# Optimization experiments

Hardware: AMD Instinct MI355X
Metric: run time of the kernel (lower is better)

Reference implementation:

```python
import jax, jax.numpy as jnp
import numpy as np


def setup_inputs() -> dict:
    key = jax.random.key(0)
    k1, k2 = jax.random.split(key)
    # [1, D, H, W, C] cubic feature volume
    image_features = jax.random.normal(k1, (1, 64, 64, 64, 64), dtype=jnp.float32)
    # [1, N, 3] vertex coords in the original 128^3 volume, in [0, 128)
    graph_features = jax.random.uniform(k2, (1, 200000, 3), dtype=jnp.float32) * 128.0
    return {"image_features": image_features, "graph_features": graph_features}


def reference(image_features, graph_features):
    img = image_features[0]                      # [D, H, W, C]
    H = img.shape[0]
    factor = jnp.float32(128.0 / H)
    x = graph_features[..., -3] / factor         # [B, N]
    y = graph_features[..., -2] / factor
    z = graph_features[..., -1] / factor
    hm1 = jnp.float32(H - 1)
    x1 = jnp.floor(x); x2 = jnp.minimum(jnp.ceil(x), hm1)
    y1 = jnp.floor(y); y2 = jnp.minimum(jnp.ceil(y), hm1)
    z1 = jnp.floor(z); z2 = jnp.minimum(jnp.ceil(z), hm1)

    def gather(ix, iy, iz):
        # [B, N] index arrays -> [B, N, C] gathered features
        return img[ix.astype(jnp.int32), iy.astype(jnp.int32), iz.astype(jnp.int32)]

    wx = (x - x1)[..., None]; wx2 = (x2 - x)[..., None]
    wy = (y - y1)[..., None]; wy2 = (y2 - y)[..., None]
    wz = (z - z1)[..., None]; wz2 = (z2 - z)[..., None]

    # z = z1 plane
    q11 = gather(x1, y1, z1); q21 = gather(x2, y1, z1)
    q12 = gather(x1, y2, z1); q22 = gather(x2, y2, z1)
    lerp_y1 = (q22 * wx + q12 * wx2) * wy + (q21 * wx + q11 * wx2) * wy2

    # z = z2 plane
    q11 = gather(x1, y1, z2); q21 = gather(x2, y1, z2)
    q12 = gather(x1, y2, z2); q22 = gather(x2, y2, z2)
    lerp_y2 = (q22 * wx + q12 * wx2) * wy + (q21 * wx + q11 * wx2) * wy2

    return lerp_y2 * wz + lerp_y1 * wz2          # [B, N, C]
```

## Files before the change

### kernel.cpp

```cpp
#include <hip/hip_runtime.h>


#define NBUCK   4096
#define CAP     128
#define OVCAP   8192
#define HTILE_F4 1024
#define NGB     8192

typedef float __attribute__((ext_vector_type(4))) fx4;

#define GLOBAL_AS __attribute__((address_space(1)))
#define LDS_AS    __attribute__((address_space(3)))

__device__ __forceinline__ void async_copy16(const float4* g, float4* l) {
    __builtin_amdgcn_global_load_lds(
        (const GLOBAL_AS unsigned int*)(const void*)g,
        (LDS_AS unsigned int*)(void*)l, 16, 0, 0);
}

__device__ __forceinline__ float4 f4mul(float4 a, float s) {
    return make_float4(a.x * s, a.y * s, a.z * s, a.w * s);
}
__device__ __forceinline__ float4 f4fma(float4 a, float s, float4 acc) {
    return make_float4(fmaf(a.x, s, acc.x), fmaf(a.y, s, acc.y),
                       fmaf(a.z, s, acc.z), fmaf(a.w, s, acc.w));
}

__global__ __launch_bounds__(256) void scatter_kernel(
    const float* __restrict__ coords, int* __restrict__ counts,
    float4* __restrict__ buckets, float4* __restrict__ overflow, int n)
{
    int p = blockIdx.x * 256 + threadIdx.x;
    if (p >= n) return;
    float xs = coords[3 * p + 0] * 0.5f;
    float ys = coords[3 * p + 1] * 0.5f;
    float zs = coords[3 * p + 2] * 0.5f;
    int vx = (int)floorf(xs), vy = (int)floorf(ys), vz = (int)floorf(zs);
    int bucket = ((vx >> 2) << 8) | ((vy >> 2) << 4) | (vz >> 2);
    int slot = atomicAdd(&counts[bucket], 1);
    float4 v = make_float4(xs, ys, zs, __int_as_float(p));
    if (slot < CAP) {
        buckets[bucket * CAP + slot] = v;
    } else {
        int o = atomicAdd(&counts[NBUCK], 1);
        if (o < OVCAP) overflow[o] = v;
    }
}

__device__ __forceinline__ void lerp_lds_half(
    const float4* __restrict__ cur, float4 cs,
    int bx0, int by0, int bz0, int cvec, int chbase,
    float* __restrict__ out)
{
    float x = cs.x, y = cs.y, z = cs.z;
    int p = __float_as_int(cs.w);

    float fx1 = floorf(x), fx2 = fminf(ceilf(x), 63.0f);
    float fy1 = floorf(y), fy2 = fminf(ceilf(y), 63.0f);
    float fz1 = floorf(z), fz2 = fminf(ceilf(z), 63.0f);

    int ax1 = ((int)fx1 - bx0) * 25, ax2 = ((int)fx2 - bx0) * 25;
    int ay1 = ((int)fy1 - by0) * 5,  ay2 = ((int)fy2 - by0) * 5;
    int lz1 = (int)fz1 - bz0,        lz2 = (int)fz2 - bz0;

    float wx = x - fx1, wxc = fx2 - x;
    float wy = y - fy1, wyc = fy2 - y;
    float wz = z - fz1, wzc = fz2 - z;

    float4 q11 = cur[((ax1 + ay1 + lz1) << 3) + cvec];
    float4 q21 = cur[((ax2 + ay1 + lz1) << 3) + cvec];
    float4 q12 = cur[((ax1 + ay2 + lz1) << 3) + cvec];
    float4 q22 = cur[((ax2 + ay2 + lz1) << 3) + cvec];
    float4 ly1v = f4fma(f4fma(q22, wx, f4mul(q12, wxc)), wy,
                        f4mul(f4fma(q21, wx, f4mul(q11, wxc)), wyc));
    q11 = cur[((ax1 + ay1 + lz2) << 3) + cvec];
    q21 = cur[((ax2 + ay1 + lz2) << 3) + cvec];
    q12 = cur[((ax1 + ay2 + lz2) << 3) + cvec];
    q22 = cur[((ax2 + ay2 + lz2) << 3) + cvec];
    float4 ly2v = f4fma(f4fma(q22, wx, f4mul(q12, wxc)), wy,
                        f4mul(f4fma(q21, wx, f4mul(q11, wxc)), wyc));

    float4 res = f4fma(ly2v, wz, f4mul(ly1v, wzc));
    fx4 r; r.x = res.x; r.y = res.y; r.z = res.z; r.w = res.w;
    __builtin_nontemporal_store(r, (fx4*)out + (p << 4) + chbase + cvec);
}

__device__ __forceinline__ void lerp_global_store(
    const float4* __restrict__ imgv, float4 cs, int cvec,
    float* __restrict__ out)
{
    float x = cs.x, y = cs.y, z = cs.z;
    int p = __float_as_int(cs.w);

    float fx1 = floorf(x), fx2 = fminf(ceilf(x), 63.0f);
    float fy1 = floorf(y), fy2 = fminf(ceilf(y), 63.0f);
    float fz1 = floorf(z), fz2 = fminf(ceilf(z), 63.0f);

    int bx1 = ((int)fx1) << 12, bx2 = ((int)fx2) << 12;
    int by1 = ((int)fy1) << 6,  by2 = ((int)fy2) << 6;
    int iz1 = (int)fz1, iz2 = (int)fz2;

    float wx = x - fx1, wxc = fx2 - x;
    float wy = y - fy1, wyc = fy2 - y;
    float wz = z - fz1, wzc = fz2 - z;

    float4 q11 = imgv[((bx1 + by1 + iz1) << 4) + cvec];
    float4 q21 = imgv[((bx2 + by1 + iz1) << 4) + cvec];
    float4 q12 = imgv[((bx1 + by2 + iz1) << 4) + cvec];
    float4 q22 = imgv[((bx2 + by2 + iz1) << 4) + cvec];
    float4 ly1v = f4fma(f4fma(q22, wx, f4mul(q12, wxc)), wy,
                        f4mul(f4fma(q21, wx, f4mul(q11, wxc)), wyc));
    q11 = imgv[((bx1 + by1 + iz2) << 4) + cvec];
    q21 = imgv[((bx2 + by1 + iz2) << 4) + cvec];
    q12 = imgv[((bx1 + by2 + iz2) << 4) + cvec];
    q22 = imgv[((bx2 + by2 + iz2) << 4) + cvec];
    float4 ly2v = f4fma(f4fma(q22, wx, f4mul(q12, wxc)), wy,
                        f4mul(f4fma(q21, wx, f4mul(q11, wxc)), wyc));

    float4 res = f4fma(ly2v, wz, f4mul(ly1v, wzc));
    fx4 r; r.x = res.x; r.y = res.y; r.z = res.z; r.w = res.w;
    __builtin_nontemporal_store(r, (fx4*)out + (p << 4) + cvec);
}

__global__ __launch_bounds__(256, 8) void gather_kernel(
    const float* __restrict__ img, const int* __restrict__ counts,
    const float4* __restrict__ buckets, const float4* __restrict__ overflow,
    float* __restrict__ out)
{
    const float4* __restrict__ imgv = (const float4*)img;

    if (blockIdx.x < NGB) {
        __shared__ float4 tile[HTILE_F4];
        int cvec = threadIdx.x & 7;
        int grp  = threadIdx.x >> 3;
        int wv   = threadIdx.x >> 6;
        int lane = threadIdx.x & 63;

        int seq    = (blockIdx.x & 7) * 1024 + (blockIdx.x >> 3);
        int bucket = seq >> 1;
        int half   = seq & 1;
        int chbase = half << 3;
        int base   = bucket * CAP;
        int bx0 = (bucket >> 8) << 2;
        int by0 = ((bucket >> 4) & 15) << 2;
        int bz0 = (bucket & 15) << 2;

        int cnt = counts[bucket];
        float4 cs0 = buckets[base + grp];
        float4 cs1 = buckets[base + grp + 32];

        #pragma unroll
        for (int c = 0; c < 4; c++) {
            int chunk = (wv << 2) + c;
            int f = chunk * 64 + lane;
            int tv = min(f >> 3, 124);
            int ch = f & 7;
            int lx = tv / 25;
            int rem = tv - lx * 25;
            int ly = rem / 5;
            int lz = rem - ly * 5;
            int gx = min(bx0 + lx, 63);
            int gy = min(by0 + ly, 63);
            int gz = min(bz0 + lz, 63);
            const float4* src =
                &imgv[(((((gx << 6) + gy) << 6) + gz) << 4) + chbase + ch];
            async_copy16(src, &tile[chunk * 64]);
        }
        cnt = min(cnt, CAP);

        __syncthreads();

        if (grp < cnt)
            lerp_lds_half(tile, cs0, bx0, by0, bz0, cvec, chbase, out);
        if (grp + 32 < cnt)
            lerp_lds_half(tile, cs1, bx0, by0, bz0, cvec, chbase, out);
        for (int t = grp + 64; t < cnt; t += 32) {
            float4 cs = buckets[base + t];
            lerp_lds_half(tile, cs, bx0, by0, bz0, cvec, chbase, out);
        }
    } else {
        int cvec = threadIdx.x & 15;
        int grp  = threadIdx.x >> 4;
        int ob = blockIdx.x - NGB;
        int cnt = min(counts[NBUCK], OVCAP);
        for (int i = (ob << 4) + grp; i < cnt; i += 32 * 16) {
            float4 cs = overflow[i];
            lerp_global_store(imgv, cs, cvec, out);
        }
    }
}

__global__ __launch_bounds__(256) void trilerp_kernel(
    const float* __restrict__ img, const float* __restrict__ coords,
    float* __restrict__ out, int n_points)
{
    int tid = blockIdx.x * 256 + threadIdx.x;
    int p = tid >> 4;
    if (p >= n_points) return;
    int cvec = tid & 15;

    float x = coords[3 * p + 0] * 0.5f;
    float y = coords[3 * p + 1] * 0.5f;
    float z = coords[3 * p + 2] * 0.5f;

    float4 cs = make_float4(x, y, z, __int_as_float(p));
    lerp_global_store((const float4*)img, cs, cvec, out);
}

extern "C" void kernel_launch(void* const* d_in, const int* in_sizes, int n_in,
                              void* d_out, int out_size, void* d_ws, size_t ws_size,
                              hipStream_t stream) {
    const float* img    = (const float*)d_in[0];
    const float* coords = (const float*)d_in[1];
    float* out = (float*)d_out;
    int n = in_sizes[1] / 3;

    size_t counts_bytes = 32768;
    size_t buckets_off  = counts_bytes;
    size_t buckets_bytes = (size_t)NBUCK * CAP * sizeof(float4);
    size_t overflow_off = buckets_off + buckets_bytes;
    size_t need = overflow_off + (size_t)OVCAP * sizeof(float4);

    if (ws_size >= need) {
        int*    counts   = (int*)d_ws;
        float4* buckets  = (float4*)((char*)d_ws + buckets_off);
        float4* overflow = (float4*)((char*)d_ws + overflow_off);

        hipMemsetAsync(counts, 0, (NBUCK + 1) * sizeof(int), stream);
        int pgrid = (n + 255) / 256;
        scatter_kernel<<<pgrid, 256, 0, stream>>>(coords, counts, buckets, overflow, n);
        gather_kernel<<<NGB + 32, 256, 0, stream>>>(img, counts, buckets, overflow, out);
    } else {
        int threads = n * 16;
        int grid = (threads + 255) / 256;
        trilerp_kernel<<<grid, 256, 0, stream>>>(img, coords, out, n);
    }
}
```

Measured before the change: 140.2 us.

## Enlarge spatial buckets to 8^3 voxels with quarter-channel LDS tiles

Points are now binned into 512 buckets of 8^3 voxels instead of 4096 buckets of 4^3. Each 512-thread block loads a 9^3-voxel halo tile for a quarter of the channels into LDS, about 46 KB. The aim is to cut redundant halo reads of the feature volume: the halo ratio drops from 125/64 to 729/512, which lowers global memory traffic for the tile loads. In exchange, fewer and larger blocks use more LDS each, occupancy drops, and there is less overlap between the tile-load phase and the compute phase.

```diff
diff --git a/kernel.cpp b/kernel.cpp
--- a/kernel.cpp
+++ b/kernel.cpp
@@ -1,11 +1,11 @@
 #include <hip/hip_runtime.h>
 
 
-#define NBUCK   4096
-#define CAP     128
+#define NB8     512
+#define CAP8    640
 #define OVCAP   8192
-#define HTILE_F4 1024
-#define NGB     8192
+#define TILE8_F4 2944
+#define NGB     2048
 
 typedef float __attribute__((ext_vector_type(4))) fx4;
 
@@ -36,18 +36,18 @@
     float ys = coords[3 * p + 1] * 0.5f;
     float zs = coords[3 * p + 2] * 0.5f;
     int vx = (int)floorf(xs), vy = (int)floorf(ys), vz = (int)floorf(zs);
-    int bucket = ((vx >> 2) << 8) | ((vy >> 2) << 4) | (vz >> 2);
+    int bucket = ((vx >> 3) << 6) | ((vy >> 3) << 3) | (vz >> 3);
     int slot = atomicAdd(&counts[bucket], 1);
     float4 v = make_float4(xs, ys, zs, __int_as_float(p));
-    if (slot < CAP) {
-        buckets[bucket * CAP + slot] = v;
+    if (slot < CAP8) {
+        buckets[bucket * CAP8 + slot] = v;
     } else {
-        int o = atomicAdd(&counts[NBUCK], 1);
+        int o = atomicAdd(&counts[NB8], 1);
         if (o < OVCAP) overflow[o] = v;
     }
 }
 
-__device__ __forceinline__ void lerp_lds_half(
+__device__ __forceinline__ void lerp_lds_q(
     const float4* __restrict__ cur, float4 cs,
     int bx0, int by0, int bz0, int cvec, int chbase,
     float* __restrict__ out)
@@ -59,24 +59,24 @@
     float fy1 = floorf(y), fy2 = fminf(ceilf(y), 63.0f);
     float fz1 = floorf(z), fz2 = fminf(ceilf(z), 63.0f);
 
-    int ax1 = ((int)fx1 - bx0) * 25, ax2 = ((int)fx2 - bx0) * 25;
-    int ay1 = ((int)fy1 - by0) * 5,  ay2 = ((int)fy2 - by0) * 5;
+    int ax1 = ((int)fx1 - bx0) * 81, ax2 = ((int)fx2 - bx0) * 81;
+    int ay1 = ((int)fy1 - by0) * 9,  ay2 = ((int)fy2 - by0) * 9;
     int lz1 = (int)fz1 - bz0,        lz2 = (int)fz2 - bz0;
 
     float wx = x - fx1, wxc = fx2 - x;
     float wy = y - fy1, wyc = fy2 - y;
     float wz = z - fz1, wzc = fz2 - z;
 
-    float4 q11 = cur[((ax1 + ay1 + lz1) << 3) + cvec];
-    float4 q21 = cur[((ax2 + ay1 + lz1) << 3) + cvec];
-    float4 q12 = cur[((ax1 + ay2 + lz1) << 3) + cvec];
-    float4 q22 = cur[((ax2 + ay2 + lz1) << 3) + cvec];
+    float4 q11 = cur[((ax1 + ay1 + lz1) << 2) + cvec];
+    float4 q21 = cur[((ax2 + ay1 + lz1) << 2) + cvec];
+    float4 q12 = cur[((ax1 + ay2 + lz1) << 2) + cvec];
+    float4 q22 = cur[((ax2 + ay2 + lz1) << 2) + cvec];
     float4 ly1v = f4fma(f4fma(q22, wx, f4mul(q12, wxc)), wy,
                         f4mul(f4fma(q21, wx, f4mul(q11, wxc)), wyc));
-    q11 = cur[((ax1 + ay1 + lz2) << 3) + cvec];
-    q21 = cur[((ax2 + ay1 + lz2) << 3) + cvec];
-    q12 = cur[((ax1 + ay2 + lz2) << 3) + cvec];
-    q22 = cur[((ax2 + ay2 + lz2) << 3) + cvec];
+    q11 = cur[((ax1 + ay1 + lz2) << 2) + cvec];
+    q21 = cur[((ax2 + ay1 + lz2) << 2) + cvec];
+    q12 = cur[((ax1 + ay2 + lz2) << 2) + cvec];
+    q22 = cur[((ax2 + ay2 + lz2) << 2) + cvec];
     float4 ly2v = f4fma(f4fma(q22, wx, f4mul(q12, wxc)), wy,
                         f4mul(f4fma(q21, wx, f4mul(q11, wxc)), wyc));
 
@@ -122,7 +122,7 @@
     __builtin_nontemporal_store(r, (fx4*)out + (p << 4) + cvec);
 }
 
-__global__ __launch_bounds__(256, 8) void gather_kernel(
+__global__ __launch_bounds__(512, 4) void gather_kernel(
     const float* __restrict__ img, const int* __restrict__ counts,
     const float4* __restrict__ buckets, const float4* __restrict__ overflow,
     float* __restrict__ out)
@@ -130,60 +130,65 @@
     const float4* __restrict__ imgv = (const float4*)img;
 
     if (blockIdx.x < NGB) {
-        __shared__ float4 tile[HTILE_F4];
-        int cvec = threadIdx.x & 7;
-        int grp  = threadIdx.x >> 3;
+        __shared__ float4 tile[TILE8_F4];
+        int cvec = threadIdx.x & 3;
+        int grp  = threadIdx.x >> 2;
         int wv   = threadIdx.x >> 6;
         int lane = threadIdx.x & 63;
 
-        int seq    = (blockIdx.x & 7) * 1024 + (blockIdx.x >> 3);
-        int bucket = seq >> 1;
-        int half   = seq & 1;
-        int chbase = half << 3;
-        int base   = bucket * CAP;
-        int bx0 = (bucket >> 8) << 2;
-        int by0 = ((bucket >> 4) & 15) << 2;
-        int bz0 = (bucket & 15) << 2;
+        int seq    = (blockIdx.x & 7) * 256 + (blockIdx.x >> 3);
+        int bucket = seq >> 2;
+        int split  = seq & 3;
+        int chbase = split << 2;
+        int base   = bucket * CAP8;
+        int bx0 = (bucket >> 6) << 3;
+        int by0 = ((bucket >> 3) & 7) << 3;
+        int bz0 = (bucket & 7) << 3;
 
         int cnt = counts[bucket];
         float4 cs0 = buckets[base + grp];
-        float4 cs1 = buckets[base + grp + 32];
+        float4 cs1 = buckets[base + grp + 128];
+        float4 cs2 = buckets[base + grp + 256];
 
         #pragma unroll
-        for (int c = 0; c < 4; c++) {
-            int chunk = (wv << 2) + c;
-            int f = chunk * 64 + lane;
-            int tv = min(f >> 3, 124);
-            int ch = f & 7;
-            int lx = tv / 25;
-            int rem = tv - lx * 25;
-            int ly = rem / 5;
-            int lz = rem - ly * 5;
-            int gx = min(bx0 + lx, 63);
-            int gy = min(by0 + ly, 63);
-            int gz = min(bz0 + lz, 63);
-            const float4* src =
-                &imgv[(((((gx << 6) + gy) << 6) + gz) << 4) + chbase + ch];
-            async_copy16(src, &tile[chunk * 64]);
+        for (int c = 0; c < 6; c++) {
+            int chunk = wv * 6 + c;
+            if (chunk < 46) {
+                int f = chunk * 64 + lane;
+                int tv = min(f >> 2, 728);
+                int ch = (f & 3) + chbase;
+                int lx = tv / 81;
+                int rem = tv - lx * 81;
+                int ly = rem / 9;
+                int lz = rem - ly * 9;
+                int gx = min(bx0 + lx, 63);
+                int gy = min(by0 + ly, 63);
+                int gz = min(bz0 + lz, 63);
+                const float4* src =
+                    &imgv[(((((gx << 6) + gy) << 6) + gz) << 4) + ch];
+                async_copy16(src, &tile[chunk * 64]);
+            }
         }
-        cnt = min(cnt, CAP);
+        cnt = min(cnt, CAP8);
 
         __syncthreads();
 
         if (grp < cnt)
-            lerp_lds_half(tile, cs0, bx0, by0, bz0, cvec, chbase, out);
-        if (grp + 32 < cnt)
-            lerp_lds_half(tile, cs1, bx0, by0, bz0, cvec, chbase, out);
-        for (int t = grp + 64; t < cnt; t += 32) {
+            lerp_lds_q(tile, cs0, bx0, by0, bz0, cvec, chbase, out);
+        if (grp + 128 < cnt)
+            lerp_lds_q(tile, cs1, bx0, by0, bz0, cvec, chbase, out);
+        if (grp + 256 < cnt)
+            lerp_lds_q(tile, cs2, bx0, by0, bz0, cvec, chbase, out);
+        for (int t = grp + 384; t < cnt; t += 128) {
             float4 cs = buckets[base + t];
-            lerp_lds_half(tile, cs, bx0, by0, bz0, cvec, chbase, out);
+            lerp_lds_q(tile, cs, bx0, by0, bz0, cvec, chbase, out);
         }
     } else {
         int cvec = threadIdx.x & 15;
         int grp  = threadIdx.x >> 4;
         int ob = blockIdx.x - NGB;
-        int cnt = min(counts[NBUCK], OVCAP);
-        for (int i = (ob << 4) + grp; i < cnt; i += 32 * 16) {
+        int cnt = min(counts[NB8], OVCAP);
+        for (int i = (ob << 5) + grp; i < cnt; i += 32 * 32) {
             float4 cs = overflow[i];
             lerp_global_store(imgv, cs, cvec, out);
         }
@@ -215,10 +220,10 @@
     float* out = (float*)d_out;
     int n = in_sizes[1] / 3;
 
-    size_t counts_bytes = 32768;
-    size_t buckets_off  = counts_bytes;
-    size_t buckets_bytes = (size_t)NBUCK * CAP * sizeof(float4);
-    size_t overflow_off = buckets_off + buckets_bytes;
+    size_t counts_bytes  = 32768;
+    size_t buckets_off   = counts_bytes;
+    size_t buckets_bytes = (size_t)NB8 * CAP8 * sizeof(float4);
+    size_t overflow_off  = buckets_off + buckets_bytes;
     size_t need = overflow_off + (size_t)OVCAP * sizeof(float4);
 
     if (ws_size >= need) {
@@ -226,10 +231,10 @@
         float4* buckets  = (float4*)((char*)d_ws + buckets_off);
         float4* overflow = (float4*)((char*)d_ws + overflow_off);
 
-        hipMemsetAsync(counts, 0, (NBUCK + 1) * sizeof(int), stream);
+        hipMemsetAsync(counts, 0, (NB8 + 1) * sizeof(int), stream);
         int pgrid = (n + 255) / 256;
         scatter_kernel<<<pgrid, 256, 0, stream>>>(coords, counts, buckets, overflow, n);
-        gather_kernel<<<NGB + 32, 256, 0, stream>>>(img, counts, buckets, overflow, out);
+        gather_kernel<<<NGB + 32, 512, 0, stream>>>(img, counts, buckets, overflow, out);
     } else {
         int threads = n * 16;
         int grid = (threads + 255) / 256;
```

Result: slower. 197.9 us (+41.1%).
